# Kernel optimization log

Hardware: AMD Instinct MI355X
Metric: run time of the kernel (lower is better)

## Reference

```python
import jax, jax.numpy as jnp
import numpy as np

DIM_Q = 512
DIM_K = 512
D_Q4 = float(DIM_Q) ** 0.25  # torch: dim_q ** (1/4)
D_K4 = float(DIM_K) ** 0.25


def setup_inputs() -> dict:
    key = jax.random.key(0)
    ks = jax.random.split(key, 9)
    B, N, D_IN = 8, 4096, 512
    s_in = 1.0 / np.sqrt(D_IN)
    return {
        "x_q": jax.random.normal(ks[0], (B, N, D_IN), jnp.float32),
        "x_k": jax.random.normal(ks[1], (B, N, D_IN), jnp.float32),
        "x_v": jax.random.normal(ks[2], (B, N, D_IN), jnp.float32),
        # Linear params stored as [in, out] for x @ W + b
        "W_q": jax.random.uniform(ks[3], (D_IN, DIM_Q), jnp.float32, -s_in, s_in),
        "b_q": jax.random.uniform(ks[4], (DIM_Q,), jnp.float32, -s_in, s_in),
        "W_k": jax.random.uniform(ks[5], (D_IN, DIM_K), jnp.float32, -s_in, s_in),
        "b_k": jax.random.uniform(ks[6], (DIM_K,), jnp.float32, -s_in, s_in),
        "W_v": jax.random.uniform(ks[7], (D_IN, DIM_K), jnp.float32, -s_in, s_in),
        "b_v": jax.random.uniform(ks[8], (DIM_K,), jnp.float32, -s_in, s_in),
    }


def reference(x_q, x_k, x_v, W_q, b_q, W_k, b_k, W_v, b_v):
    Q = x_q @ W_q + b_q          # [B, n, dq]
    K = x_k @ W_k + b_k          # [B, n, dk]
    V = x_v @ W_v + b_v          # [B, n, dk]
    # softmax_row: over sequence axis (dim=-2) of Q
    A = jax.nn.softmax(Q / D_Q4, axis=-2)          # [B, n, dq]
    # softmax_col on K^T (dim=-1) == softmax over sequence axis of K
    Ks = jax.nn.softmax(K / D_K4, axis=-2)         # [B, n, dk]
    Bm = jnp.einsum("bnd,bne->bde", Ks, V)        # [B, dk, dk]
    Z = jnp.einsum("bnd,bde->bne", A, Bm)         # [B, n, dk]
    return Z
```

## Files before the change

### kernel.cpp

```cpp
#include <hip/hip_runtime.h>
#include <hip/hip_bf16.h>


typedef __bf16 bf16_t;
typedef __attribute__((ext_vector_type(8))) __bf16 bf16x8;
typedef __attribute__((ext_vector_type(4))) float f32x4;

#define MFMA_BF16 __builtin_amdgcn_mfma_f32_16x16x32_bf16

__device__ inline void async_ld16(const void* g, void* l) {
  __builtin_amdgcn_global_load_lds(
      (const __attribute__((address_space(1))) void*)g,
      (__attribute__((address_space(3))) void*)l, 16, 0, 0);
}

#define INV_D4 0.2102241038134287f

#define BAR_LGKM()                                        \
  do {                                                    \
    asm volatile("s_waitcnt lgkmcnt(0)" ::: "memory");    \
    __builtin_amdgcn_s_barrier();                         \
  } while (0)

#define BAR_VM_LGKM()                                             \
  do {                                                            \
    asm volatile("s_waitcnt vmcnt(0) lgkmcnt(0)" ::: "memory");   \
    __builtin_amdgcn_s_barrier();                                 \
  } while (0)

__device__ inline void cvt_store(bf16_t* dst, int c0, int ar, const float4& f0,
                                 const float4& f1, const float4& f2,
                                 const float4& f3) {
  bf16x8 p0, p1;
  p0[0] = (__bf16)f0.x; p0[1] = (__bf16)f0.y; p0[2] = (__bf16)f0.z; p0[3] = (__bf16)f0.w;
  p0[4] = (__bf16)f1.x; p0[5] = (__bf16)f1.y; p0[6] = (__bf16)f1.z; p0[7] = (__bf16)f1.w;
  p1[0] = (__bf16)f2.x; p1[1] = (__bf16)f2.y; p1[2] = (__bf16)f2.z; p1[3] = (__bf16)f2.w;
  p1[4] = (__bf16)f3.x; p1[5] = (__bf16)f3.y; p1[6] = (__bf16)f3.z; p1[7] = (__bf16)f3.w;
  ((bf16x8*)dst)[c0 * 128 + ar] = p0;
  ((bf16x8*)dst)[(c0 + 1) * 128 + ar] = p1;
}

__global__ __launch_bounds__(256) void wt_kernel(
    const float* __restrict__ Wq, const float* __restrict__ Wk,
    const float* __restrict__ Wv, bf16_t* __restrict__ Wt) {
  const int z = blockIdx.z;
  const float* W = (z == 0) ? Wq : (z == 1) ? Wk : Wv;
  bf16_t* O = Wt + (size_t)z * 262144;
  __shared__ __align__(16) bf16_t tile[64 * 72];
  const int t = threadIdx.x;
  const int r = t >> 2;
  const int c4 = (t & 3) * 16;
  const int in0 = blockIdx.x * 64, out0 = blockIdx.y * 64;
  const float* src = W + (size_t)(in0 + r) * 512 + out0 + c4;
#pragma unroll
  for (int i = 0; i < 4; ++i) {
    float4 f = ((const float4*)src)[i];
    tile[(c4 + i * 4 + 0) * 72 + r] = (__bf16)f.x;
    tile[(c4 + i * 4 + 1) * 72 + r] = (__bf16)f.y;
    tile[(c4 + i * 4 + 2) * 72 + r] = (__bf16)f.z;
    tile[(c4 + i * 4 + 3) * 72 + r] = (__bf16)f.w;
  }
  __syncthreads();
  bf16x8* dst = (bf16x8*)(O + (size_t)(out0 + r) * 512 + in0 + c4);
  const bf16x8* s = (const bf16x8*)(tile + r * 72 + c4);
  dst[0] = s[0];
  dst[1] = s[1];
}

__global__ __launch_bounds__(256, 2) void proj_q(
    const float* __restrict__ Xq, const bf16_t* __restrict__ Wt,
    const float* __restrict__ bias, bf16_t* __restrict__ Eq,
    float* __restrict__ Sq) {
  __shared__ __align__(16) bf16_t Xs[2][4096];

  const int t = threadIdx.x;
  const int lane = t & 63, w = t >> 6;
  const int quad = lane >> 4, l15 = lane & 15;
  const int m0 = blockIdx.x * 128;
  const int n0 = blockIdx.y * 256 + w * 64;

  f32x4 acc[8][4];
  const f32x4 zero4 = {0.f, 0.f, 0.f, 0.f};
#pragma unroll
  for (int i = 0; i < 8; ++i)
#pragma unroll
    for (int j = 0; j < 4; ++j) acc[i][j] = zero4;

  const int ar = t >> 1;
  const int c0 = (t & 1) * 2;
  const float* abase = Xq + (size_t)(m0 + ar) * 512 + (t & 1) * 16;
  const bf16_t* wbase = Wt + (size_t)(n0 + l15) * 512 + quad * 8;

  float4 fb[2][4];
  bf16x8 wr[2][4];

  {
    const float4* p = (const float4*)abase;
    fb[1][0] = p[0]; fb[1][1] = p[1]; fb[1][2] = p[2]; fb[1][3] = p[3];
  }
#pragma unroll
  for (int ni = 0; ni < 4; ++ni)
    wr[0][ni] = *(const bf16x8*)(wbase + ni * 8192);
  {
    const float4* p = (const float4*)(abase + 32);
    fb[0][0] = p[0]; fb[0][1] = p[1]; fb[0][2] = p[2]; fb[0][3] = p[3];
  }
  cvt_store(Xs[0], c0, ar, fb[1][0], fb[1][1], fb[1][2], fb[1][3]);
  {
    const float4* p = (const float4*)(abase + 64);
    fb[1][0] = p[0]; fb[1][1] = p[1]; fb[1][2] = p[2]; fb[1][3] = p[3];
  }
  BAR_LGKM();

#pragma unroll
  for (int ks = 0; ks < 16; ++ks) {
    const int p = ks & 1;
    bf16x8 af[8];
#pragma unroll
    for (int mi = 0; mi < 8; ++mi)
      af[mi] = ((const bf16x8*)Xs[p])[quad * 128 + mi * 16 + l15];
    if (ks < 15) {
      cvt_store(Xs[p ^ 1], c0, ar, fb[p][0], fb[p][1], fb[p][2], fb[p][3]);
#pragma unroll
      for (int ni = 0; ni < 4; ++ni)
        wr[p ^ 1][ni] = *(const bf16x8*)(wbase + ni * 8192 + (ks + 1) * 32);
      if (ks < 13) {
        const float4* pp = (const float4*)(abase + (ks + 3) * 32);
        fb[p][0] = pp[0]; fb[p][1] = pp[1]; fb[p][2] = pp[2]; fb[p][3] = pp[3];
      }
    }
#pragma unroll
    for (int mi = 0; mi < 8; ++mi)
#pragma unroll
      for (int ni = 0; ni < 4; ++ni)
        acc[mi][ni] = MFMA_BF16(af[mi], wr[p][ni], acc[mi][ni], 0, 0, 0);
    if (ks < 15) BAR_LGKM();
  }

  const int b = m0 >> 12;
  float cs[4] = {0.f, 0.f, 0.f, 0.f};
#pragma unroll
  for (int ni = 0; ni < 4; ++ni) {
    const int col = n0 + ni * 16 + l15;
    const float bv_ = bias[col];
#pragma unroll
    for (int mi = 0; mi < 8; ++mi)
#pragma unroll
      for (int r = 0; r < 4; ++r) {
        const int row = m0 + mi * 16 + quad * 4 + r;
        float v = __expf((acc[mi][ni][r] + bv_) * INV_D4);
        Eq[(size_t)row * 512 + col] = (bf16_t)v;
        cs[ni] += v;
      }
  }
#pragma unroll
  for (int ni = 0; ni < 4; ++ni) {
    cs[ni] += __shfl_xor(cs[ni], 16);
    cs[ni] += __shfl_xor(cs[ni], 32);
  }
  if (lane < 16) {
#pragma unroll
    for (int ni = 0; ni < 4; ++ni)
      atomicAdd(&Sq[b * 512 + n0 + ni * 16 + lane], cs[ni]);
  }
}

__global__ __launch_bounds__(256, 2) void proj_kv(
    const float* __restrict__ xk, const float* __restrict__ xv,
    const bf16_t* __restrict__ Wt, const float* __restrict__ bk,
    const float* __restrict__ bv, bf16_t* __restrict__ Ft,
    bf16_t* __restrict__ Vt) {
  const int z = blockIdx.z + 1;
  const float* X = (z == 1) ? xk : xv;
  const float* bias = (z == 1) ? bk : bv;
  const bf16_t* W = Wt + (size_t)z * 262144;
  bf16_t* Out = (z == 1) ? Ft : Vt;
  const bool expm = (z == 1);

  __shared__ __align__(16) bf16_t Xs[2][4096];

  const int t = threadIdx.x;
  const int lane = t & 63, w = t >> 6;
  const int quad = lane >> 4, l15 = lane & 15;
  const int ng = blockIdx.x * 128;
  const int d0 = blockIdx.y * 256 + w * 64;

  f32x4 acc[4][8];
  const f32x4 zero4 = {0.f, 0.f, 0.f, 0.f};
#pragma unroll
  for (int i = 0; i < 4; ++i)
#pragma unroll
    for (int j = 0; j < 8; ++j) acc[i][j] = zero4;

  const int ar = t >> 1;
  const int c0 = (t & 1) * 2;
  const float* bbase = X + (size_t)(ng + ar) * 512 + (t & 1) * 16;
  const bf16_t* wbase = W + (size_t)(d0 + l15) * 512 + quad * 8;

  float4 fb[2][4];
  bf16x8 wr[2][4];

  {
    const float4* p = (const float4*)bbase;
    fb[1][0] = p[0]; fb[1][1] = p[1]; fb[1][2] = p[2]; fb[1][3] = p[3];
  }
#pragma unroll
  for (int mi = 0; mi < 4; ++mi)
    wr[0][mi] = *(const bf16x8*)(wbase + mi * 8192);
  {
    const float4* p = (const float4*)(bbase + 32);
    fb[0][0] = p[0]; fb[0][1] = p[1]; fb[0][2] = p[2]; fb[0][3] = p[3];
  }
  cvt_store(Xs[0], c0, ar, fb[1][0], fb[1][1], fb[1][2], fb[1][3]);
  {
    const float4* p = (const float4*)(bbase + 64);
    fb[1][0] = p[0]; fb[1][1] = p[1]; fb[1][2] = p[2]; fb[1][3] = p[3];
  }
  BAR_LGKM();

#pragma unroll
  for (int ks = 0; ks < 16; ++ks) {
    const int p = ks & 1;
    bf16x8 bx[8];
#pragma unroll
    for (int ni = 0; ni < 8; ++ni)
      bx[ni] = ((const bf16x8*)Xs[p])[quad * 128 + ni * 16 + l15];
    if (ks < 15) {
      cvt_store(Xs[p ^ 1], c0, ar, fb[p][0], fb[p][1], fb[p][2], fb[p][3]);
#pragma unroll
      for (int mi = 0; mi < 4; ++mi)
        wr[p ^ 1][mi] = *(const bf16x8*)(wbase + mi * 8192 + (ks + 1) * 32);
      if (ks < 13) {
        const float4* pp = (const float4*)(bbase + (ks + 3) * 32);
        fb[p][0] = pp[0]; fb[p][1] = pp[1]; fb[p][2] = pp[2]; fb[p][3] = pp[3];
      }
    }
#pragma unroll
    for (int mi = 0; mi < 4; ++mi)
#pragma unroll
      for (int ni = 0; ni < 8; ++ni)
        acc[mi][ni] = MFMA_BF16(wr[p][mi], bx[ni], acc[mi][ni], 0, 0, 0);
    if (ks < 15) BAR_LGKM();
  }

  const int b = ng >> 12;
  const int nl0 = (ng & 4095);
#pragma unroll
  for (int mi = 0; mi < 4; ++mi)
#pragma unroll
    for (int r = 0; r < 4; ++r) {
      const int d = d0 + mi * 16 + quad * 4 + r;
      const float bv_ = bias[d];
      bf16_t* rowp = Out + (size_t)b * 2097152 + (size_t)d * 4096 + nl0;
#pragma unroll
      for (int ni = 0; ni < 8; ++ni) {
        float v = acc[mi][ni][r] + bv_;
        if (expm) v = __expf(v * INV_D4);
        rowp[ni * 16 + l15] = (bf16_t)v;
      }
    }
}

__global__ __launch_bounds__(256) void sk_kernel(const bf16_t* __restrict__ Ft,
                                                 float* __restrict__ Sk) {
  const int row = blockIdx.x * 4 + (threadIdx.x >> 6);
  const int lane = threadIdx.x & 63;
  const bf16x8* p = (const bf16x8*)(Ft + (size_t)row * 4096) + lane;
  float s = 0.f;
#pragma unroll
  for (int j = 0; j < 8; ++j) {
    bf16x8 v = p[j * 64];
#pragma unroll
    for (int e = 0; e < 8; ++e) s += (float)v[e];
  }
#pragma unroll
  for (int m = 1; m <= 32; m <<= 1) s += __shfl_xor(s, m);
  if (lane == 0) Sk[row] = s;
}

__global__ __launch_bounds__(256, 2) void bm_gemm(
    const bf16_t* __restrict__ Ft, const bf16_t* __restrict__ Vt,
    float* __restrict__ Bmp, int S) {
  const int b = blockIdx.z / S;
  const int s = blockIdx.z - b * S;
  const int d0 = blockIdx.x * 128;
  const int e0 = blockIdx.y * 128;
  const bf16_t* A = Ft + (size_t)b * 2097152;
  const bf16_t* B = Vt + (size_t)b * 2097152;
  float* out = Bmp + ((size_t)s * 8 + b) * 262144;

  __shared__ __align__(16) bf16_t As[2][4096];
  __shared__ __align__(16) bf16_t Bs[2][4096];

  const int t = threadIdx.x;
  const int lane = t & 63, w = t >> 6;
  const int quad = lane >> 4, l15 = lane & 15;
  const int m_off = (w & 1) * 64, n_off = (w >> 1) * 64;

  const int kper = 4096 / S;
  const int KS = kper >> 5;
  const int kbase = s * kper;

  f32x4 acc[4][4];
  const f32x4 zero4 = {0.f, 0.f, 0.f, 0.f};
#pragma unroll
  for (int i = 0; i < 4; ++i)
#pragma unroll
    for (int j = 0; j < 4; ++j) acc[i][j] = zero4;

  const int j0 = w * 2;
  auto stage = [&](int buf, int ks) {
#pragma unroll
    for (int i = 0; i < 2; ++i) {
      const int j = j0 + i;
      const int k8 = j >> 1;
      const int r = ((j & 1) << 6) + lane;
      const int kel = kbase + ks * 32 + k8 * 8;
      async_ld16(A + (size_t)(d0 + r) * 4096 + kel, &As[buf][j * 512]);
      async_ld16(B + (size_t)(e0 + r) * 4096 + kel, &Bs[buf][j * 512]);
    }
  };

  stage(0, 0);
  BAR_VM_LGKM();

  for (int ks = 0; ks < KS; ++ks) {
    const int p = ks & 1;
    if (ks + 1 < KS) stage(p ^ 1, ks + 1);
    bf16x8 af[4], bfr[4];
#pragma unroll
    for (int mi = 0; mi < 4; ++mi)
      af[mi] = ((const bf16x8*)As[p])[quad * 128 + m_off + mi * 16 + l15];
#pragma unroll
    for (int ni = 0; ni < 4; ++ni)
      bfr[ni] = ((const bf16x8*)Bs[p])[quad * 128 + n_off + ni * 16 + l15];
#pragma unroll
    for (int mi = 0; mi < 4; ++mi)
#pragma unroll
      for (int ni = 0; ni < 4; ++ni)
        acc[mi][ni] = MFMA_BF16(af[mi], bfr[ni], acc[mi][ni], 0, 0, 0);
    if (ks + 1 < KS) BAR_VM_LGKM();
  }

#pragma unroll
  for (int mi = 0; mi < 4; ++mi)
#pragma unroll
    for (int ni = 0; ni < 4; ++ni) {
      const int ecol = e0 + n_off + ni * 16 + l15;
#pragma unroll
      for (int r = 0; r < 4; ++r) {
        const int drow = d0 + m_off + mi * 16 + quad * 4 + r;
        out[(size_t)drow * 512 + ecol] = acc[mi][ni][r];
      }
    }
}

__global__ __launch_bounds__(256) void scale_kernel(
    const float* __restrict__ Bmp, const float* __restrict__ Sq,
    const float* __restrict__ Sk, bf16_t* __restrict__ Ct, int S) {
  const int b = blockIdx.z;
  const int d0 = blockIdx.x * 64, e0 = blockIdx.y * 64;
  __shared__ __align__(16) bf16_t tile[64 * 72];
  const int t = threadIdx.x;
  const int r = t >> 2;
  const int c4 = (t & 3) * 16;
  const int d = d0 + r;
  const float f = 1.0f / (Sq[b * 512 + d] * Sk[b * 512 + d]);
  const float* p0 = Bmp + (size_t)b * 262144 + (size_t)d * 512 + e0 + c4;
#pragma unroll
  for (int i = 0; i < 4; ++i) {
    float sx = 0.f, sy = 0.f, sz = 0.f, sw = 0.f;
    for (int sp = 0; sp < S; ++sp) {
      float4 v = ((const float4*)(p0 + (size_t)sp * 2097152))[i];
      sx += v.x; sy += v.y; sz += v.z; sw += v.w;
    }
    tile[(c4 + i * 4 + 0) * 72 + r] = (__bf16)(sx * f);
    tile[(c4 + i * 4 + 1) * 72 + r] = (__bf16)(sy * f);
    tile[(c4 + i * 4 + 2) * 72 + r] = (__bf16)(sz * f);
    tile[(c4 + i * 4 + 3) * 72 + r] = (__bf16)(sw * f);
  }
  __syncthreads();
  bf16x8* dst = (bf16x8*)(Ct + (size_t)b * 262144 + (size_t)(e0 + r) * 512 + d0 + c4);
  const bf16x8* sptr = (const bf16x8*)(tile + r * 72 + c4);
  dst[0] = sptr[0];
  dst[1] = sptr[1];
}

__global__ __launch_bounds__(256, 2) void z_gemm(
    const bf16_t* __restrict__ Eq, const bf16_t* __restrict__ Ct,
    float* __restrict__ out) {
  __shared__ __align__(16) bf16_t Xs[2][4096];

  const int t = threadIdx.x;
  const int lane = t & 63, w = t >> 6;
  const int quad = lane >> 4, l15 = lane & 15;
  const int m0 = blockIdx.x * 128;
  const int n0 = blockIdx.y * 256 + w * 64;
  const int batch = m0 >> 12;
  const bf16_t* Bt = Ct + (size_t)batch * 262144;

  f32x4 acc[8][4];
  const f32x4 zero4 = {0.f, 0.f, 0.f, 0.f};
#pragma unroll
  for (int i = 0; i < 8; ++i)
#pragma unroll
    for (int j = 0; j < 4; ++j) acc[i][j] = zero4;

  const int ar = t >> 1;
  const int c0 = (t & 1) * 2;
  const bf16_t* abase = Eq + (size_t)(m0 + ar) * 512 + (t & 1) * 16;
  const bf16_t* wbase = Bt + (size_t)(n0 + l15) * 512 + quad * 8;

  bf16x8 eb[2][2];
  bf16x8 wr[2][4];

  eb[1][0] = *(const bf16x8*)abase;
  eb[1][1] = *(const bf16x8*)(abase + 8);
#pragma unroll
  for (int ni = 0; ni < 4; ++ni)
    wr[0][ni] = *(const bf16x8*)(wbase + ni * 8192);
  eb[0][0] = *(const bf16x8*)(abase + 32);
  eb[0][1] = *(const bf16x8*)(abase + 40);
  ((bf16x8*)Xs[0])[c0 * 128 + ar] = eb[1][0];
  ((bf16x8*)Xs[0])[(c0 + 1) * 128 + ar] = eb[1][1];
  eb[1][0] = *(const bf16x8*)(abase + 64);
  eb[1][1] = *(const bf16x8*)(abase + 72);
  BAR_LGKM();

#pragma unroll
  for (int ks = 0; ks < 16; ++ks) {
    const int p = ks & 1;
    bf16x8 af[8];
#pragma unroll
    for (int mi = 0; mi < 8; ++mi)
      af[mi] = ((const bf16x8*)Xs[p])[quad * 128 + mi * 16 + l15];
    if (ks < 15) {
      ((bf16x8*)Xs[p ^ 1])[c0 * 128 + ar] = eb[p][0];
      ((bf16x8*)Xs[p ^ 1])[(c0 + 1) * 128 + ar] = eb[p][1];
#pragma unroll
      for (int ni = 0; ni < 4; ++ni)
        wr[p ^ 1][ni] = *(const bf16x8*)(wbase + ni * 8192 + (ks + 1) * 32);
      if (ks < 13) {
        eb[p][0] = *(const bf16x8*)(abase + (ks + 3) * 32);
        eb[p][1] = *(const bf16x8*)(abase + (ks + 3) * 32 + 8);
      }
    }
#pragma unroll
    for (int mi = 0; mi < 8; ++mi)
#pragma unroll
      for (int ni = 0; ni < 4; ++ni)
        acc[mi][ni] = MFMA_BF16(af[mi], wr[p][ni], acc[mi][ni], 0, 0, 0);
    if (ks < 15) BAR_LGKM();
  }

#pragma unroll
  for (int mi = 0; mi < 8; ++mi)
#pragma unroll
    for (int ni = 0; ni < 4; ++ni) {
      const int col = n0 + ni * 16 + l15;
#pragma unroll
      for (int r = 0; r < 4; ++r) {
        const int row = m0 + mi * 16 + quad * 4 + r;
        out[(size_t)row * 512 + col] = acc[mi][ni][r];
      }
    }
}

extern "C" void kernel_launch(void* const* d_in, const int* in_sizes, int n_in,
                              void* d_out, int out_size, void* d_ws,
                              size_t ws_size, hipStream_t stream) {
  const float* xq = (const float*)d_in[0];
  const float* xk = (const float*)d_in[1];
  const float* xv = (const float*)d_in[2];
  const float* Wq = (const float*)d_in[3];
  const float* bq = (const float*)d_in[4];
  const float* Wk = (const float*)d_in[5];
  const float* bk = (const float*)d_in[6];
  const float* Wv = (const float*)d_in[7];
  const float* bv = (const float*)d_in[8];
  float* out = (float*)d_out;

  char* ws = (char*)d_ws;
  bf16_t* Eq = (bf16_t*)(ws + 0);
  bf16_t* Ft = (bf16_t*)(ws + 33554432);
  bf16_t* Vt = (bf16_t*)(ws + 67108864);
  float* Bmp = (float*)(ws + 100663296);

  const int S = (ws_size >= (size_t)135823360) ? 4 : 2;
  const size_t wt_off = (S == 4) ? (size_t)134217728 : (size_t)117440512;
  bf16_t* Wt = (bf16_t*)(ws + wt_off);
  float* Sq = (float*)(ws + wt_off + 1572864);
  float* Sk = (float*)(ws + wt_off + 1572864 + 16384);
  bf16_t* Ct = (bf16_t*)(ws + 33554432);

  hipMemsetAsync(Sq, 0, 16384, stream);

  wt_kernel<<<dim3(8, 8, 3), 256, 0, stream>>>(Wq, Wk, Wv, Wt);
  proj_q<<<dim3(256, 2), 256, 0, stream>>>(xq, Wt, bq, Eq, Sq);
  proj_kv<<<dim3(256, 2, 2), 256, 0, stream>>>(xk, xv, Wt, bk, bv, Ft, Vt);
  sk_kernel<<<dim3(1024), 256, 0, stream>>>(Ft, Sk);
  bm_gemm<<<dim3(4, 4, 8 * S), 256, 0, stream>>>(Ft, Vt, Bmp, S);
  scale_kernel<<<dim3(8, 8, 8), 256, 0, stream>>>(Bmp, Sq, Sk, Ct, S);
  z_gemm<<<dim3(256, 2), 256, 0, stream>>>(Eq, Ct, out);
}
```

Baseline: 378.0 us.

## Coalesce projection loads, deepen K tiles with XOR-swizzled LDS in bmm and z_gemm

The projection kernels now have each thread load contiguous float4s across 8 threads per row instead of 4 strided float4s per thread. They also pad the LDS layout (132-stride) to avoid bank conflicts. The Bm reduction GEMM and z_gemm switch to 64-wide K tiles staged with async global→LDS loads and an XOR-swizzled row layout, which halves the barrier count and removes the register round-trip. In exchange LDS use doubles, which may reduce occupancy, and z_gemm now loads its weight fragments directly without prefetch.

```diff
diff --git a/kernel.cpp b/kernel.cpp
--- a/kernel.cpp
+++ b/kernel.cpp
@@ -4,6 +4,7 @@
 
 typedef __bf16 bf16_t;
 typedef __attribute__((ext_vector_type(8))) __bf16 bf16x8;
+typedef __attribute__((ext_vector_type(4))) __bf16 bf16x4;
 typedef __attribute__((ext_vector_type(4))) float f32x4;
 
 #define MFMA_BF16 __builtin_amdgcn_mfma_f32_16x16x32_bf16
@@ -28,16 +29,15 @@
     __builtin_amdgcn_s_barrier();                                 \
   } while (0)
 
-__device__ inline void cvt_store(bf16_t* dst, int c0, int ar, const float4& f0,
-                                 const float4& f1, const float4& f2,
-                                 const float4& f3) {
-  bf16x8 p0, p1;
-  p0[0] = (__bf16)f0.x; p0[1] = (__bf16)f0.y; p0[2] = (__bf16)f0.z; p0[3] = (__bf16)f0.w;
-  p0[4] = (__bf16)f1.x; p0[5] = (__bf16)f1.y; p0[6] = (__bf16)f1.z; p0[7] = (__bf16)f1.w;
-  p1[0] = (__bf16)f2.x; p1[1] = (__bf16)f2.y; p1[2] = (__bf16)f2.z; p1[3] = (__bf16)f2.w;
-  p1[4] = (__bf16)f3.x; p1[5] = (__bf16)f3.y; p1[6] = (__bf16)f3.z; p1[7] = (__bf16)f3.w;
-  ((bf16x8*)dst)[c0 * 128 + ar] = p0;
-  ((bf16x8*)dst)[(c0 + 1) * 128 + ar] = p1;
+__device__ inline void cvt_store4(bf16_t* dst, const float4* f, int cch,
+                                  int xr, int half) {
+#pragma unroll
+  for (int i = 0; i < 4; ++i) {
+    bf16x4 v;
+    v[0] = (__bf16)f[i].x; v[1] = (__bf16)f[i].y;
+    v[2] = (__bf16)f[i].z; v[3] = (__bf16)f[i].w;
+    *(bf16x4*)(dst + (size_t)(cch * 132 + xr + 32 * i) * 8 + half * 4) = v;
+  }
 }
 
 __global__ __launch_bounds__(256) void wt_kernel(
@@ -71,7 +71,7 @@
     const float* __restrict__ Xq, const bf16_t* __restrict__ Wt,
     const float* __restrict__ bias, bf16_t* __restrict__ Eq,
     float* __restrict__ Sq) {
-  __shared__ __align__(16) bf16_t Xs[2][4096];
+  __shared__ __align__(16) bf16_t Xs[2][4224];
 
   const int t = threadIdx.x;
   const int lane = t & 63, w = t >> 6;
@@ -86,30 +86,27 @@
 #pragma unroll
     for (int j = 0; j < 4; ++j) acc[i][j] = zero4;
 
-  const int ar = t >> 1;
-  const int c0 = (t & 1) * 2;
-  const float* abase = Xq + (size_t)(m0 + ar) * 512 + (t & 1) * 16;
+  const int xr = t >> 3;
+  const int f4 = t & 7;
+  const int cch = f4 >> 1, half = f4 & 1;
+  const float* abase = Xq + (size_t)(m0 + xr) * 512 + f4 * 4;
   const bf16_t* wbase = Wt + (size_t)(n0 + l15) * 512 + quad * 8;
 
   float4 fb[2][4];
   bf16x8 wr[2][4];
 
-  {
-    const float4* p = (const float4*)abase;
-    fb[1][0] = p[0]; fb[1][1] = p[1]; fb[1][2] = p[2]; fb[1][3] = p[3];
-  }
+#pragma unroll
+  for (int i = 0; i < 4; ++i) fb[1][i] = *(const float4*)(abase + i * 16384);
 #pragma unroll
   for (int ni = 0; ni < 4; ++ni)
     wr[0][ni] = *(const bf16x8*)(wbase + ni * 8192);
-  {
-    const float4* p = (const float4*)(abase + 32);
-    fb[0][0] = p[0]; fb[0][1] = p[1]; fb[0][2] = p[2]; fb[0][3] = p[3];
-  }
-  cvt_store(Xs[0], c0, ar, fb[1][0], fb[1][1], fb[1][2], fb[1][3]);
-  {
-    const float4* p = (const float4*)(abase + 64);
-    fb[1][0] = p[0]; fb[1][1] = p[1]; fb[1][2] = p[2]; fb[1][3] = p[3];
-  }
+#pragma unroll
+  for (int i = 0; i < 4; ++i)
+    fb[0][i] = *(const float4*)(abase + i * 16384 + 32);
+  cvt_store4(Xs[0], fb[1], cch, xr, half);
+#pragma unroll
+  for (int i = 0; i < 4; ++i)
+    fb[1][i] = *(const float4*)(abase + i * 16384 + 64);
   BAR_LGKM();
 
 #pragma unroll
@@ -118,15 +115,16 @@
     bf16x8 af[8];
 #pragma unroll
     for (int mi = 0; mi < 8; ++mi)
-      af[mi] = ((const bf16x8*)Xs[p])[quad * 128 + mi * 16 + l15];
+      af[mi] = *(const bf16x8*)(&Xs[p][(size_t)(quad * 132 + mi * 16 + l15) * 8]);
     if (ks < 15) {
-      cvt_store(Xs[p ^ 1], c0, ar, fb[p][0], fb[p][1], fb[p][2], fb[p][3]);
+      cvt_store4(Xs[p ^ 1], fb[p], cch, xr, half);
 #pragma unroll
       for (int ni = 0; ni < 4; ++ni)
         wr[p ^ 1][ni] = *(const bf16x8*)(wbase + ni * 8192 + (ks + 1) * 32);
       if (ks < 13) {
-        const float4* pp = (const float4*)(abase + (ks + 3) * 32);
-        fb[p][0] = pp[0]; fb[p][1] = pp[1]; fb[p][2] = pp[2]; fb[p][3] = pp[3];
+#pragma unroll
+        for (int i = 0; i < 4; ++i)
+          fb[p][i] = *(const float4*)(abase + i * 16384 + (ks + 3) * 32);
       }
     }
 #pragma unroll
@@ -177,7 +175,7 @@
   bf16_t* Out = (z == 1) ? Ft : Vt;
   const bool expm = (z == 1);
 
-  __shared__ __align__(16) bf16_t Xs[2][4096];
+  __shared__ __align__(16) bf16_t Xs[2][4224];
 
   const int t = threadIdx.x;
   const int lane = t & 63, w = t >> 6;
@@ -192,30 +190,27 @@
 #pragma unroll
     for (int j = 0; j < 8; ++j) acc[i][j] = zero4;
 
-  const int ar = t >> 1;
-  const int c0 = (t & 1) * 2;
-  const float* bbase = X + (size_t)(ng + ar) * 512 + (t & 1) * 16;
+  const int xr = t >> 3;
+  const int f4 = t & 7;
+  const int cch = f4 >> 1, half = f4 & 1;
+  const float* bbase = X + (size_t)(ng + xr) * 512 + f4 * 4;
   const bf16_t* wbase = W + (size_t)(d0 + l15) * 512 + quad * 8;
 
   float4 fb[2][4];
   bf16x8 wr[2][4];
 
-  {
-    const float4* p = (const float4*)bbase;
-    fb[1][0] = p[0]; fb[1][1] = p[1]; fb[1][2] = p[2]; fb[1][3] = p[3];
-  }
+#pragma unroll
+  for (int i = 0; i < 4; ++i) fb[1][i] = *(const float4*)(bbase + i * 16384);
 #pragma unroll
   for (int mi = 0; mi < 4; ++mi)
     wr[0][mi] = *(const bf16x8*)(wbase + mi * 8192);
-  {
-    const float4* p = (const float4*)(bbase + 32);
-    fb[0][0] = p[0]; fb[0][1] = p[1]; fb[0][2] = p[2]; fb[0][3] = p[3];
-  }
-  cvt_store(Xs[0], c0, ar, fb[1][0], fb[1][1], fb[1][2], fb[1][3]);
-  {
-    const float4* p = (const float4*)(bbase + 64);
-    fb[1][0] = p[0]; fb[1][1] = p[1]; fb[1][2] = p[2]; fb[1][3] = p[3];
-  }
+#pragma unroll
+  for (int i = 0; i < 4; ++i)
+    fb[0][i] = *(const float4*)(bbase + i * 16384 + 32);
+  cvt_store4(Xs[0], fb[1], cch, xr, half);
+#pragma unroll
+  for (int i = 0; i < 4; ++i)
+    fb[1][i] = *(const float4*)(bbase + i * 16384 + 64);
   BAR_LGKM();
 
 #pragma unroll
@@ -224,15 +219,16 @@
     bf16x8 bx[8];
 #pragma unroll
     for (int ni = 0; ni < 8; ++ni)
-      bx[ni] = ((const bf16x8*)Xs[p])[quad * 128 + ni * 16 + l15];
+      bx[ni] = *(const bf16x8*)(&Xs[p][(size_t)(quad * 132 + ni * 16 + l15) * 8]);
     if (ks < 15) {
-      cvt_store(Xs[p ^ 1], c0, ar, fb[p][0], fb[p][1], fb[p][2], fb[p][3]);
+      cvt_store4(Xs[p ^ 1], fb[p], cch, xr, half);
 #pragma unroll
       for (int mi = 0; mi < 4; ++mi)
         wr[p ^ 1][mi] = *(const bf16x8*)(wbase + mi * 8192 + (ks + 1) * 32);
       if (ks < 13) {
-        const float4* pp = (const float4*)(bbase + (ks + 3) * 32);
-        fb[p][0] = pp[0]; fb[p][1] = pp[1]; fb[p][2] = pp[2]; fb[p][3] = pp[3];
+#pragma unroll
+        for (int i = 0; i < 4; ++i)
+          fb[p][i] = *(const float4*)(bbase + i * 16384 + (ks + 3) * 32);
       }
     }
 #pragma unroll
@@ -289,8 +285,8 @@
   const bf16_t* B = Vt + (size_t)b * 2097152;
   float* out = Bmp + ((size_t)s * 8 + b) * 262144;
 
-  __shared__ __align__(16) bf16_t As[2][4096];
-  __shared__ __align__(16) bf16_t Bs[2][4096];
+  __shared__ __align__(16) bf16_t As[2][8192];
+  __shared__ __align__(16) bf16_t Bs[2][8192];
 
   const int t = threadIdx.x;
   const int lane = t & 63, w = t >> 6;
@@ -298,7 +294,7 @@
   const int m_off = (w & 1) * 64, n_off = (w >> 1) * 64;
 
   const int kper = 4096 / S;
-  const int KS = kper >> 5;
+  const int KS = kper >> 6;
   const int kbase = s * kper;
 
   f32x4 acc[4][4];
@@ -308,16 +304,19 @@
 #pragma unroll
     for (int j = 0; j < 4; ++j) acc[i][j] = zero4;
 
-  const int j0 = w * 2;
+  const int srow = lane >> 3;
+  const int spiece = (lane & 7) ^ srow;
+  const bf16_t* asrc = A + (size_t)(d0 + srow) * 4096 + kbase + spiece * 8;
+  const bf16_t* bsrc = B + (size_t)(e0 + srow) * 4096 + kbase + spiece * 8;
+  const int q0 = w * 4;
+  const int rsw = l15 & 7;
+
   auto stage = [&](int buf, int ks) {
 #pragma unroll
-    for (int i = 0; i < 2; ++i) {
-      const int j = j0 + i;
-      const int k8 = j >> 1;
-      const int r = ((j & 1) << 6) + lane;
-      const int kel = kbase + ks * 32 + k8 * 8;
-      async_ld16(A + (size_t)(d0 + r) * 4096 + kel, &As[buf][j * 512]);
-      async_ld16(B + (size_t)(e0 + r) * 4096 + kel, &Bs[buf][j * 512]);
+    for (int i = 0; i < 4; ++i) {
+      const int q = q0 + i;
+      async_ld16(asrc + (size_t)q * 8 * 4096 + ks * 64, &As[buf][q * 512]);
+      async_ld16(bsrc + (size_t)q * 8 * 4096 + ks * 64, &Bs[buf][q * 512]);
     }
   };
 
@@ -327,18 +326,26 @@
   for (int ks = 0; ks < KS; ++ks) {
     const int p = ks & 1;
     if (ks + 1 < KS) stage(p ^ 1, ks + 1);
-    bf16x8 af[4], bfr[4];
-#pragma unroll
-    for (int mi = 0; mi < 4; ++mi)
-      af[mi] = ((const bf16x8*)As[p])[quad * 128 + m_off + mi * 16 + l15];
-#pragma unroll
-    for (int ni = 0; ni < 4; ++ni)
-      bfr[ni] = ((const bf16x8*)Bs[p])[quad * 128 + n_off + ni * 16 + l15];
-#pragma unroll
-    for (int mi = 0; mi < 4; ++mi)
-#pragma unroll
-      for (int ni = 0; ni < 4; ++ni)
-        acc[mi][ni] = MFMA_BF16(af[mi], bfr[ni], acc[mi][ni], 0, 0, 0);
+#pragma unroll
+    for (int ksub = 0; ksub < 2; ++ksub) {
+      const int c = ksub * 4 + quad;
+      bf16x8 af[4], bfr[4];
+#pragma unroll
+      for (int mi = 0; mi < 4; ++mi) {
+        const int row = m_off + mi * 16 + l15;
+        af[mi] = *(const bf16x8*)(&As[p][(size_t)row * 64 + ((c ^ rsw) << 3)]);
+      }
+#pragma unroll
+      for (int ni = 0; ni < 4; ++ni) {
+        const int row = n_off + ni * 16 + l15;
+        bfr[ni] = *(const bf16x8*)(&Bs[p][(size_t)row * 64 + ((c ^ rsw) << 3)]);
+      }
+#pragma unroll
+      for (int mi = 0; mi < 4; ++mi)
+#pragma unroll
+        for (int ni = 0; ni < 4; ++ni)
+          acc[mi][ni] = MFMA_BF16(af[mi], bfr[ni], acc[mi][ni], 0, 0, 0);
+    }
     if (ks + 1 < KS) BAR_VM_LGKM();
   }
 
@@ -389,7 +396,7 @@
 __global__ __launch_bounds__(256, 2) void z_gemm(
     const bf16_t* __restrict__ Eq, const bf16_t* __restrict__ Ct,
     float* __restrict__ out) {
-  __shared__ __align__(16) bf16_t Xs[2][4096];
+  __shared__ __align__(16) bf16_t As[2][8192];
 
   const int t = threadIdx.x;
   const int lane = t & 63, w = t >> 6;
@@ -406,51 +413,51 @@
 #pragma unroll
     for (int j = 0; j < 4; ++j) acc[i][j] = zero4;
 
-  const int ar = t >> 1;
-  const int c0 = (t & 1) * 2;
-  const bf16_t* abase = Eq + (size_t)(m0 + ar) * 512 + (t & 1) * 16;
+  const int srow = lane >> 3;
+  const int spiece = (lane & 7) ^ srow;
+  const bf16_t* asrc = Eq + (size_t)(m0 + srow) * 512 + spiece * 8;
+  const int q0 = w * 4;
+  const int rsw = l15 & 7;
   const bf16_t* wbase = Bt + (size_t)(n0 + l15) * 512 + quad * 8;
 
-  bf16x8 eb[2][2];
-  bf16x8 wr[2][4];
-
-  eb[1][0] = *(const bf16x8*)abase;
-  eb[1][1] = *(const bf16x8*)(abase + 8);
-#pragma unroll
-  for (int ni = 0; ni < 4; ++ni)
-    wr[0][ni] = *(const bf16x8*)(wbase + ni * 8192);
-  eb[0][0] = *(const bf16x8*)(abase + 32);
-  eb[0][1] = *(const bf16x8*)(abase + 40);
-  ((bf16x8*)Xs[0])[c0 * 128 + ar] = eb[1][0];
-  ((bf16x8*)Xs[0])[(c0 + 1) * 128 + ar] = eb[1][1];
-  eb[1][0] = *(const bf16x8*)(abase + 64);
-  eb[1][1] = *(const bf16x8*)(abase + 72);
-  BAR_LGKM();
-
-#pragma unroll
-  for (int ks = 0; ks < 16; ++ks) {
+  auto stageZ = [&](int buf, int ks) {
+#pragma unroll
+    for (int i = 0; i < 4; ++i) {
+      const int q = q0 + i;
+      async_ld16(asrc + (size_t)q * 8 * 512 + ks * 64, &As[buf][q * 512]);
+    }
+  };
+
+  stageZ(0, 0);
+  BAR_VM_LGKM();
+
+#pragma unroll
+  for (int ks = 0; ks < 8; ++ks) {
     const int p = ks & 1;
-    bf16x8 af[8];
-#pragma unroll
-    for (int mi = 0; mi < 8; ++mi)
-      af[mi] = ((const bf16x8*)Xs[p])[quad * 128 + mi * 16 + l15];
-    if (ks < 15) {
-      ((bf16x8*)Xs[p ^ 1])[c0 * 128 + ar] = eb[p][0];
-      ((bf16x8*)Xs[p ^ 1])[(c0 + 1) * 128 + ar] = eb[p][1];
-#pragma unroll
-      for (int ni = 0; ni < 4; ++ni)
-        wr[p ^ 1][ni] = *(const bf16x8*)(wbase + ni * 8192 + (ks + 1) * 32);
-      if (ks < 13) {
-        eb[p][0] = *(const bf16x8*)(abase + (ks + 3) * 32);
-        eb[p][1] = *(const bf16x8*)(abase + (ks + 3) * 32 + 8);
-      }
-    }
-#pragma unroll
-    for (int mi = 0; mi < 8; ++mi)
-#pragma unroll
-      for (int ni = 0; ni < 4; ++ni)
-        acc[mi][ni] = MFMA_BF16(af[mi], wr[p][ni], acc[mi][ni], 0, 0, 0);
-    if (ks < 15) BAR_LGKM();
+    if (ks < 7) stageZ(p ^ 1, ks + 1);
+    bf16x8 wrA[4], wrB[4];
+#pragma unroll
+    for (int ni = 0; ni < 4; ++ni) {
+      wrA[ni] = *(const bf16x8*)(wbase + ni * 8192 + ks * 64);
+      wrB[ni] = *(const bf16x8*)(wbase + ni * 8192 + ks * 64 + 32);
+    }
+#pragma unroll
+    for (int ksub = 0; ksub < 2; ++ksub) {
+      const int c = ksub * 4 + quad;
+      bf16x8 af[8];
+#pragma unroll
+      for (int mi = 0; mi < 8; ++mi) {
+        const int row = mi * 16 + l15;
+        af[mi] = *(const bf16x8*)(&As[p][(size_t)row * 64 + ((c ^ rsw) << 3)]);
+      }
+#pragma unroll
+      for (int mi = 0; mi < 8; ++mi)
+#pragma unroll
+        for (int ni = 0; ni < 4; ++ni)
+          acc[mi][ni] =
+              MFMA_BF16(af[mi], ksub ? wrB[ni] : wrA[ni], acc[mi][ni], 0, 0, 0);
+    }
+    if (ks < 7) BAR_VM_LGKM();
   }
 
 #pragma unroll
```

After: 357.2 us. 1.06x faster.
